# Optimization experiments

Measured on AMD Instinct MI355X. Metric: run time of the kernel, lower is better.

## Reference

```python
import jax, jax.numpy as jnp
import numpy as np

N_COUNTIES = 3144
P = 2
N_MOB = 6
N_COV = 10
T = 156
NNZ = 31440


def setup_inputs() -> dict:
    key = jax.random.key(0)
    ks = jax.random.split(key, 13)
    C = jax.random.uniform(ks[0], (T, N_COUNTIES), dtype=jnp.float32)
    D = jax.random.uniform(ks[1], (T, N_COUNTIES), dtype=jnp.float32)
    M = jax.random.uniform(ks[2], (N_MOB, T, N_COUNTIES), dtype=jnp.float32)
    cov = jax.random.normal(ks[3], (N_COV, N_COUNTIES), dtype=jnp.float32)
    B_nonzero = jax.random.normal(ks[4], (NNZ,), dtype=jnp.float32)
    A_nonzero = jax.random.normal(ks[5], (NNZ,), dtype=jnp.float32)
    H_nonzero = jax.random.normal(ks[6], (NNZ,), dtype=jnp.float32)
    mu = jax.random.normal(ks[7], (N_MOB, P), dtype=jnp.float32)
    nu = jax.random.normal(ks[8], (N_MOB, P), dtype=jnp.float32)
    upsilon = jax.random.normal(ks[9], (N_COV,), dtype=jnp.float32)
    zeta = jax.random.normal(ks[10], (N_COV,), dtype=jnp.float32)
    rows = jax.random.randint(ks[11], (NNZ,), 0, N_COUNTIES)
    cols = jax.random.randint(ks[12], (NNZ,), 0, N_COUNTIES)
    return dict(C=C, D=D, M=M, cov=cov, B_nonzero=B_nonzero, A_nonzero=A_nonzero,
                H_nonzero=H_nonzero, mu=mu, nu=nu, upsilon=upsilon, zeta=zeta,
                rows=rows, cols=cols)


def reference(C, D, M, cov, B_nonzero, A_nonzero, H_nonzero, mu, nu, upsilon, zeta, rows, cols):
    n = C.shape[1]
    p = mu.shape[1]
    Tp = C.shape[0] - p  # number of predicted steps (t = p .. T-1)

    # Dense scatter-built weight matrices (duplicates summed, matching
    # torch.sparse .to_dense()). The torch code reuses the SAME nonzero
    # vector for every lag tau, so B[tau] == B for all tau.
    B = jnp.zeros((n, n), C.dtype).at[rows, cols].add(B_nonzero)
    A = jnp.zeros((n, n), C.dtype).at[rows, cols].add(A_nonzero)
    H = jnp.zeros((n, n), C.dtype).at[rows, cols].add(H_nonzero)

    # Lagged windows: Cl[tau, i] = C[i + tau] == C[t - p + tau] for t = p + i.
    Cl = jnp.stack([C[tau:tau + Tp] for tau in range(p)], 0)  # [p, Tp, n]
    Dl = jnp.stack([D[tau:tau + Tp] for tau in range(p)], 0)  # [p, Tp, n]
    Ml = jnp.stack([M[:, tau:tau + Tp, :] for tau in range(p)], 1)  # [n_mob, p, Tp, n]

    # Since B[tau] are identical across lags, sum over p folds into one GEMM.
    c2c = jnp.einsum('ptn,nm->tm', Cl, B)  # [Tp, n]
    c2d = jnp.einsum('ptn,nm->tm', Cl, H)
    d2d = jnp.einsum('ptn,nm->tm', Dl, A)

    mob_c = jnp.einsum('kptn,kp->tn', Ml, mu)
    mob_d = jnp.einsum('kptn,kp->tn', Ml, nu)

    C_hat = c2c + mob_c + upsilon @ cov  # [Tp, n] (+ broadcast [n])
    D_hat = c2d + d2d + mob_d + zeta @ cov
    return C_hat, D_hat
```

## Files before the change

kernel.cpp:

```cpp
#include <hip/hip_runtime.h>


#define BS      256
#define ECAP    64
#define SPILLC  4096
#define SCAN_TH 1024

__global__ void prep(const int* __restrict__ rows, const int* __restrict__ cols,
                     const float* __restrict__ Bnz, const float* __restrict__ Anz,
                     const float* __restrict__ Hnz,
                     const float* __restrict__ C, const float* __restrict__ D,
                     float* __restrict__ Ct, float* __restrict__ Dt,
                     float4* __restrict__ edges, int* __restrict__ cnt,
                     int* __restrict__ spill_cnt, int* __restrict__ spill,
                     int T, int NC, int NNZ, int fillBlocks, int cT64, int tT64) {
    if ((int)blockIdx.x < fillBlocks) {
        int k = blockIdx.x * BS + threadIdx.x;
        if (k < NNZ) {
            int c = cols[k];
            int j = atomicAdd(&cnt[c], 1);
            if (j < ECAP)
                edges[(size_t)c * ECAP + j] =
                    make_float4(__int_as_float(rows[k]), Bnz[k], Anz[k], Hnz[k]);
            else {
                int sp = atomicAdd(spill_cnt, 1);
                if (sp < SPILLC) spill[sp] = k;
            }
        }
        return;
    }
    __shared__ float tile[64][65];
    int bid = blockIdx.x - fillBlocks;
    int tTiles = cT64 * tT64;
    int z = bid / tTiles;
    int r = bid - z * tTiles;
    int ct = r / tT64, tt = r - ct * tT64;
    const float* src = z ? D : C;
    float* dst = z ? Dt : Ct;
    int lx = threadIdx.x & 63, ly = threadIdx.x >> 6;
    int c0 = ct * 64, t0 = tt * 64;
    for (int rr = ly; rr < 64; rr += 4) {
        int t = t0 + rr, c = c0 + lx;
        if (t < T && c < NC) tile[rr][lx] = src[(size_t)t * NC + c];
    }
    __syncthreads();
    for (int rr = ly; rr < 64; rr += 4) {
        int c = c0 + rr, t = t0 + lx;
        if (c < NC && t < T) dst[(size_t)c * T + t] = tile[lx][rr];
    }
}

__global__ void sparse_wave(const float* __restrict__ Ct, const float* __restrict__ Dt,
                            const int* __restrict__ cnt, const float4* __restrict__ edges,
                            float* __restrict__ wsS0, float* __restrict__ wsS1,
                            int T, int TPn, int nChunks, int nWaves) {
    int gtid = blockIdx.x * blockDim.x + threadIdx.x;
    int wid = gtid >> 6, lane = threadIdx.x & 63;
    if (wid >= nWaves) return;
    int c = wid / nChunks;
    int chunk = wid - c * nChunks;
    int i = chunk * 64 + lane;
    bool valid = i < TPn;
    int isafe = valid ? i : 0;
    float a0 = 0.f, a1 = 0.f;
    int n = cnt[c]; if (n > ECAP) n = ECAP;
    const float4* eb = edges + (size_t)c * ECAP;
    for (int j = 0; j < n; ++j) {
        float4 E = eb[j];
        int g = __float_as_int(E.x);
        const float* cr = Ct + (size_t)g * T;
        const float* dr = Dt + (size_t)g * T;
        float cs = cr[isafe] + cr[isafe + 1];
        float ds = dr[isafe] + dr[isafe + 1];
        a0 += cs * E.y;
        a1 += cs * E.w + ds * E.z;
    }
    if (valid) {
        wsS0[(size_t)c * TPn + i] = a0;
        wsS1[(size_t)c * TPn + i] = a1;
    }
}

#define FTI 32
#define FTC 32
__global__ void final_fuse(const float* __restrict__ wsS0, const float* __restrict__ wsS1,
                           const float* __restrict__ M,
                           const float* __restrict__ cov,
                           const float* __restrict__ mu,
                           const float* __restrict__ nu,
                           const float* __restrict__ ups, const float* __restrict__ zet,
                           const float* __restrict__ Ct, const float* __restrict__ Dt,
                           const int* __restrict__ rows, const int* __restrict__ cols,
                           const float* __restrict__ Bnz, const float* __restrict__ Anz,
                           const float* __restrict__ Hnz,
                           const int* __restrict__ spill_cnt, const int* __restrict__ spill,
                           float* __restrict__ out0, float* __restrict__ out1,
                           int T, int NC, int NMOB, int NCOV, int TPn, int cTiles) {
    __shared__ float s0[FTI][FTC + 1], s1[FTI][FTC + 1];
    int bi = blockIdx.x / cTiles;
    int bc = blockIdx.x - bi * cTiles;
    int i0 = bi * FTI, c0 = bc * FTC;
    int tid = threadIdx.x;

    {
        int li = tid & 31;
        int lc0 = tid >> 5;
        int i = i0 + li;
        for (int cc = lc0; cc < FTC; cc += 8) {
            int c = c0 + cc;
            float v0 = 0.f, v1 = 0.f;
            if (c < NC && i < TPn) {
                v0 = wsS0[(size_t)c * TPn + i];
                v1 = wsS1[(size_t)c * TPn + i];
            }
            s0[li][cc] = v0;
            s1[li][cc] = v1;
        }
    }
    __syncthreads();

    int lc = tid & 31;
    int ri = tid >> 5;
    int c = c0 + lc;
    if (c < NC) {
        float cv0 = 0.f, cv1 = 0.f;
        for (int j = 0; j < NCOV; ++j) {
            float cv = cov[(size_t)j * NC + c];
            cv0 += cv * ups[j];
            cv1 += cv * zet[j];
        }
        for (int ii = ri; ii < FTI; ii += 8) {
            int i = i0 + ii;
            if (i >= TPn) break;
            float a0 = s0[ii][lc] + cv0;
            float a1 = s1[ii][lc] + cv1;
            for (int k = 0; k < NMOB; ++k) {
                const float* mb = M + (size_t)k * T * NC;
                float m0 = mb[(size_t)i * NC + c];
                float m1 = mb[(size_t)(i + 1) * NC + c];
                a0 += m0 * mu[k * 2] + m1 * mu[k * 2 + 1];
                a1 += m0 * nu[k * 2] + m1 * nu[k * 2 + 1];
            }
            out0[(size_t)i * NC + c] = a0;
            out1[(size_t)i * NC + c] = a1;
        }
    }

    int nsp = *spill_cnt;
    if (nsp > 0) {
        __syncthreads();
        if (nsp > SPILLC) nsp = SPILLC;
        int cmax = NC - c0; if (cmax > FTC) cmax = FTC;
        if (tid < FTI) {
            int io = i0 + tid;
            if (io < TPn) {
                for (int s = 0; s < nsp; ++s) {
                    int k = spill[s];
                    int cc = cols[k];
                    if (cc >= c0 && cc < c0 + cmax) {
                        int g = rows[k];
                        float cs = Ct[(size_t)g * T + io] + Ct[(size_t)g * T + io + 1];
                        float ds = Dt[(size_t)g * T + io] + Dt[(size_t)g * T + io + 1];
                        atomicAdd(&out0[(size_t)io * NC + cc], cs * Bnz[k]);
                        atomicAdd(&out1[(size_t)io * NC + cc], cs * Hnz[k] + ds * Anz[k]);
                    }
                }
            }
        }
    }
}

__global__ void csr_hist(const int* __restrict__ cols, int* __restrict__ counts, int NNZ) {
    int k = blockIdx.x * blockDim.x + threadIdx.x;
    if (k < NNZ) atomicAdd(&counts[cols[k]], 1);
}
__global__ __launch_bounds__(SCAN_TH)
void csr_scan(const int* __restrict__ counts, int* __restrict__ offsets,
              int* __restrict__ cursor, int NC) {
    __shared__ int ssum[SCAN_TH];
    int t = threadIdx.x;
    int chunk = (NC + SCAN_TH - 1) / SCAN_TH;
    int beg = t * chunk, end = min(beg + chunk, NC);
    int local = 0;
    for (int j = beg; j < end; ++j) local += counts[j];
    ssum[t] = local;
    __syncthreads();
    for (int off = 1; off < SCAN_TH; off <<= 1) {
        int v = (t >= off) ? ssum[t - off] : 0;
        __syncthreads();
        ssum[t] += v;
        __syncthreads();
    }
    int run = ssum[t] - local;
    for (int j = beg; j < end; ++j) {
        offsets[j] = run;
        cursor[j]  = run;
        run += counts[j];
    }
    if (t == SCAN_TH - 1) offsets[NC] = ssum[SCAN_TH - 1];
}
__global__ void csr_fill(const int* __restrict__ rows, const int* __restrict__ cols,
                         const float* __restrict__ Bnz, const float* __restrict__ Anz,
                         const float* __restrict__ Hnz,
                         int* __restrict__ cursor, float4* __restrict__ edges, int NNZ) {
    int k = blockIdx.x * blockDim.x + threadIdx.x;
    if (k >= NNZ) return;
    int s = cols[k];
    int pos = atomicAdd(&cursor[s], 1);
    edges[pos] = make_float4(__int_as_float(rows[k]), Bnz[k], Anz[k], Hnz[k]);
}
__global__ void fused_generic(const float* __restrict__ C, const float* __restrict__ D,
                              const float* __restrict__ M, const float* __restrict__ cov,
                              const float* __restrict__ mu, const float* __restrict__ nu,
                              const float* __restrict__ ups, const float* __restrict__ zet,
                              const int* __restrict__ offsets, const float4* __restrict__ edges,
                              float* __restrict__ out0, float* __restrict__ out1,
                              int T, int NC, int NMOB, int NCOV, int P, int TPn) {
    int idx = blockIdx.x * blockDim.x + threadIdx.x;
    if (idx >= TPn * NC) return;
    int i = idx / NC;
    int c = idx - i * NC;
    float acc0 = 0.f, acc1 = 0.f;
    for (int k = 0; k < NMOB; ++k)
        for (int tau = 0; tau < P; ++tau) {
            float m = M[((size_t)k * T + i + tau) * NC + c];
            acc0 += m * mu[k * P + tau];
            acc1 += m * nu[k * P + tau];
        }
    for (int j = 0; j < NCOV; ++j) {
        float cv = cov[(size_t)j * NC + c];
        acc0 += cv * ups[j];
        acc1 += cv * zet[j];
    }
    int e0 = offsets[c], e1 = offsets[c + 1];
    for (int e = e0; e < e1; ++e) {
        float4 E = edges[e];
        int g = __float_as_int(E.x);
        float cs = 0.f, ds = 0.f;
        for (int tau = 0; tau < P; ++tau) {
            cs += C[(size_t)(i + tau) * NC + g];
            ds += D[(size_t)(i + tau) * NC + g];
        }
        acc0 += cs * E.y;
        acc1 += cs * E.w + ds * E.z;
    }
    out0[idx] = acc0;
    out1[idx] = acc1;
}

extern "C" void kernel_launch(void* const* d_in, const int* in_sizes, int n_in,
                              void* d_out, int out_size, void* d_ws, size_t ws_size,
                              hipStream_t stream) {
    const float* C    = (const float*)d_in[0];
    const float* D    = (const float*)d_in[1];
    const float* M    = (const float*)d_in[2];
    const float* cov  = (const float*)d_in[3];
    const float* Bnz  = (const float*)d_in[4];
    const float* Anz  = (const float*)d_in[5];
    const float* Hnz  = (const float*)d_in[6];
    const float* mu   = (const float*)d_in[7];
    const float* nu   = (const float*)d_in[8];
    const float* ups  = (const float*)d_in[9];
    const float* zet  = (const float*)d_in[10];
    const int*  rows  = (const int*)d_in[11];
    const int*  cols  = (const int*)d_in[12];

    int NCOV = in_sizes[9];
    int NC   = in_sizes[3] / NCOV;
    int T    = in_sizes[0] / NC;
    int NMOB = in_sizes[2] / in_sizes[0];
    int P    = in_sizes[7] / NMOB;
    int NNZ  = in_sizes[11];
    int TPn  = T - P;

    float* out0 = (float*)d_out;
    float* out1 = out0 + (size_t)TPn * NC;

    float4* edges  = (float4*)d_ws;
    int*    cnt    = (int*)(edges + (size_t)NC * ECAP);
    int*    spillc = cnt + NC;
    int*    spill  = spillc + 1;
    float*  Ct     = (float*)(spill + SPILLC);
    float*  Dt     = Ct + (size_t)NC * T;
    float*  wsS0   = Dt + (size_t)NC * T;
    float*  wsS1   = wsS0 + (size_t)NC * TPn;
    size_t  need   = (size_t)((char*)(wsS1 + (size_t)NC * TPn) - (char*)d_ws);

    if (P == 2 && ws_size >= need) {
        hipMemsetAsync(cnt, 0, (size_t)(NC + 1) * sizeof(int), stream);

        int fillBlocks = (NNZ + BS - 1) / BS;
        int cT64 = (NC + 63) / 64, tT64 = (T + 63) / 64;
        prep<<<fillBlocks + 2 * cT64 * tT64, BS, 0, stream>>>(
            rows, cols, Bnz, Anz, Hnz, C, D, Ct, Dt,
            edges, cnt, spillc, spill, T, NC, NNZ, fillBlocks, cT64, tT64);

        int nChunks = (TPn + 63) / 64;
        int nWaves  = NC * nChunks;
        sparse_wave<<<(nWaves * 64 + BS - 1) / BS, BS, 0, stream>>>(
            Ct, Dt, cnt, edges, wsS0, wsS1, T, TPn, nChunks, nWaves);

        int iTiles = (TPn + FTI - 1) / FTI;
        int cTiles = (NC + FTC - 1) / FTC;
        final_fuse<<<iTiles * cTiles, BS, 0, stream>>>(
            wsS0, wsS1, M, cov, mu, nu, ups, zet, Ct, Dt,
            rows, cols, Bnz, Anz, Hnz, spillc, spill,
            out0, out1, T, NC, NMOB, NCOV, TPn, cTiles);
    } else {
        float4* fedges   = (float4*)d_ws;
        int*    foffsets = (int*)(fedges + NNZ);
        int*    fcounts  = foffsets + (NC + 1);
        int*    fcursor  = fcounts + NC;
        hipMemsetAsync(fcounts, 0, (size_t)NC * sizeof(int), stream);
        csr_hist<<<(NNZ + BS - 1) / BS, BS, 0, stream>>>(cols, fcounts, NNZ);
        csr_scan<<<1, SCAN_TH, 0, stream>>>(fcounts, foffsets, fcursor, NC);
        csr_fill<<<(NNZ + BS - 1) / BS, BS, 0, stream>>>(
            rows, cols, Bnz, Anz, Hnz, fcursor, fedges, NNZ);
        int n = TPn * NC;
        fused_generic<<<(n + BS - 1) / BS, BS, 0, stream>>>(
            C, D, M, cov, mu, nu, ups, zet, foffsets, fedges,
            out0, out1, T, NC, NMOB, NCOV, P, TPn);
    }
}
```

Baseline: 132.8 us.

## Fuse sparse gather stage into tiled final kernel, drop intermediate workspace

```diff
diff --git a/kernel.cpp b/kernel.cpp
--- a/kernel.cpp
+++ b/kernel.cpp
@@ -50,71 +50,52 @@
     }
 }
 
-__global__ void sparse_wave(const float* __restrict__ Ct, const float* __restrict__ Dt,
-                            const int* __restrict__ cnt, const float4* __restrict__ edges,
-                            float* __restrict__ wsS0, float* __restrict__ wsS1,
-                            int T, int TPn, int nChunks, int nWaves) {
-    int gtid = blockIdx.x * blockDim.x + threadIdx.x;
-    int wid = gtid >> 6, lane = threadIdx.x & 63;
-    if (wid >= nWaves) return;
-    int c = wid / nChunks;
-    int chunk = wid - c * nChunks;
-    int i = chunk * 64 + lane;
-    bool valid = i < TPn;
-    int isafe = valid ? i : 0;
-    float a0 = 0.f, a1 = 0.f;
-    int n = cnt[c]; if (n > ECAP) n = ECAP;
-    const float4* eb = edges + (size_t)c * ECAP;
-    for (int j = 0; j < n; ++j) {
-        float4 E = eb[j];
-        int g = __float_as_int(E.x);
-        const float* cr = Ct + (size_t)g * T;
-        const float* dr = Dt + (size_t)g * T;
-        float cs = cr[isafe] + cr[isafe + 1];
-        float ds = dr[isafe] + dr[isafe + 1];
-        a0 += cs * E.y;
-        a1 += cs * E.w + ds * E.z;
-    }
-    if (valid) {
-        wsS0[(size_t)c * TPn + i] = a0;
-        wsS1[(size_t)c * TPn + i] = a1;
-    }
-}
-
 #define FTI 32
 #define FTC 32
-__global__ void final_fuse(const float* __restrict__ wsS0, const float* __restrict__ wsS1,
-                           const float* __restrict__ M,
-                           const float* __restrict__ cov,
-                           const float* __restrict__ mu,
-                           const float* __restrict__ nu,
-                           const float* __restrict__ ups, const float* __restrict__ zet,
-                           const float* __restrict__ Ct, const float* __restrict__ Dt,
-                           const int* __restrict__ rows, const int* __restrict__ cols,
-                           const float* __restrict__ Bnz, const float* __restrict__ Anz,
-                           const float* __restrict__ Hnz,
-                           const int* __restrict__ spill_cnt, const int* __restrict__ spill,
-                           float* __restrict__ out0, float* __restrict__ out1,
-                           int T, int NC, int NMOB, int NCOV, int TPn, int cTiles) {
-    __shared__ float s0[FTI][FTC + 1], s1[FTI][FTC + 1];
+__global__ __launch_bounds__(BS)
+void tile_fused(const float* __restrict__ Ct,
+                const float* __restrict__ Dt,
+                const float* __restrict__ M,
+                const float* __restrict__ cov,
+                const float* __restrict__ mu,
+                const float* __restrict__ nu,
+                const float* __restrict__ ups, const float* __restrict__ zet,
+                const int* __restrict__ cnt, const float4* __restrict__ edges,
+                const int* __restrict__ rows, const int* __restrict__ cols,
+                const float* __restrict__ Bnz, const float* __restrict__ Anz,
+                const float* __restrict__ Hnz,
+                const int* __restrict__ spill_cnt, const int* __restrict__ spill,
+                float* __restrict__ out0, float* __restrict__ out1,
+                int T, int NC, int NMOB, int NCOV, int TPn, int cTiles) {
+    __shared__ float s0[FTC][FTI + 1], s1[FTC][FTI + 1];
     int bi = blockIdx.x / cTiles;
     int bc = blockIdx.x - bi * cTiles;
     int i0 = bi * FTI, c0 = bc * FTC;
     int tid = threadIdx.x;
 
     {
-        int li = tid & 31;
-        int lc0 = tid >> 5;
+        int grp = tid >> 5, li = tid & 31;
         int i = i0 + li;
-        for (int cc = lc0; cc < FTC; cc += 8) {
-            int c = c0 + cc;
-            float v0 = 0.f, v1 = 0.f;
-            if (c < NC && i < TPn) {
-                v0 = wsS0[(size_t)c * TPn + i];
-                v1 = wsS1[(size_t)c * TPn + i];
-            }
-            s0[li][cc] = v0;
-            s1[li][cc] = v1;
+        int isafe = (i < TPn) ? i : (TPn - 1);
+        for (int cl = grp; cl < FTC; cl += 8) {
+            float a0 = 0.f, a1 = 0.f;
+            int c = c0 + cl;
+            if (c < NC) {
+                int n = cnt[c]; if (n > ECAP) n = ECAP;
+                const float4* eb = edges + (size_t)c * ECAP;
+                for (int j = 0; j < n; ++j) {
+                    float4 E = eb[j];
+                    int g = __float_as_int(E.x);
+                    const float* cr = Ct + (size_t)g * T;
+                    const float* dr = Dt + (size_t)g * T;
+                    float cs = cr[isafe] + cr[isafe + 1];
+                    float ds = dr[isafe] + dr[isafe + 1];
+                    a0 += cs * E.y;
+                    a1 += cs * E.w + ds * E.z;
+                }
+            }
+            s0[cl][li] = a0;
+            s1[cl][li] = a1;
         }
     }
     __syncthreads();
@@ -132,8 +113,8 @@
         for (int ii = ri; ii < FTI; ii += 8) {
             int i = i0 + ii;
             if (i >= TPn) break;
-            float a0 = s0[ii][lc] + cv0;
-            float a1 = s1[ii][lc] + cv1;
+            float a0 = s0[lc][ii] + cv0;
+            float a1 = s1[lc][ii] + cv1;
             for (int k = 0; k < NMOB; ++k) {
                 const float* mb = M + (size_t)k * T * NC;
                 float m0 = mb[(size_t)i * NC + c];
@@ -282,9 +263,7 @@
     int*    spill  = spillc + 1;
     float*  Ct     = (float*)(spill + SPILLC);
     float*  Dt     = Ct + (size_t)NC * T;
-    float*  wsS0   = Dt + (size_t)NC * T;
-    float*  wsS1   = wsS0 + (size_t)NC * TPn;
-    size_t  need   = (size_t)((char*)(wsS1 + (size_t)NC * TPn) - (char*)d_ws);
+    size_t  need   = (size_t)((char*)(Dt + (size_t)NC * T) - (char*)d_ws);
 
     if (P == 2 && ws_size >= need) {
         hipMemsetAsync(cnt, 0, (size_t)(NC + 1) * sizeof(int), stream);
@@ -295,15 +274,10 @@
             rows, cols, Bnz, Anz, Hnz, C, D, Ct, Dt,
             edges, cnt, spillc, spill, T, NC, NNZ, fillBlocks, cT64, tT64);
 
-        int nChunks = (TPn + 63) / 64;
-        int nWaves  = NC * nChunks;
-        sparse_wave<<<(nWaves * 64 + BS - 1) / BS, BS, 0, stream>>>(
-            Ct, Dt, cnt, edges, wsS0, wsS1, T, TPn, nChunks, nWaves);
-
         int iTiles = (TPn + FTI - 1) / FTI;
         int cTiles = (NC + FTC - 1) / FTC;
-        final_fuse<<<iTiles * cTiles, BS, 0, stream>>>(
-            wsS0, wsS1, M, cov, mu, nu, ups, zet, Ct, Dt,
+        tile_fused<<<iTiles * cTiles, BS, 0, stream>>>(
+            Ct, Dt, M, cov, mu, nu, ups, zet, cnt, edges,
             rows, cols, Bnz, Anz, Hnz, spillc, spill,
             out0, out1, T, NC, NMOB, NCOV, TPn, cTiles);
     } else {
```

Result: slower. 150.4 us (+13.3%).
